# Performance work log

Measured on AMD Instinct MI355X. Metric: run time of the kernel, lower is better.

The kernel has to match this reference:

```python
import jax, jax.numpy as jnp
import numpy as np

EMBED_DIM = 1024
NUM_HEADS = 16
HEAD_DIM = EMBED_DIM // NUM_HEADS
B, S = 2, 2048


def setup_inputs() -> dict:
    key = jax.random.key(0)
    ks = jax.random.split(key, 11)
    sc = 1.0 / np.sqrt(EMBED_DIM)
    d = {
        'query': jax.random.normal(ks[0], (B, S, EMBED_DIM), jnp.float32),
        'key': jax.random.normal(ks[1], (B, S, EMBED_DIM), jnp.float32),
        'value': jax.random.normal(ks[2], (B, S, EMBED_DIM), jnp.float32),
        'Wq': jax.random.normal(ks[3], (EMBED_DIM, EMBED_DIM), jnp.float32) * sc,
        'bq': jnp.zeros((EMBED_DIM,), jnp.float32),
        'Wk': jax.random.normal(ks[4], (EMBED_DIM, EMBED_DIM), jnp.float32) * sc,
        'bk': jnp.zeros((EMBED_DIM,), jnp.float32),
        'Wv': jax.random.normal(ks[5], (EMBED_DIM, EMBED_DIM), jnp.float32) * sc,
        'bv': jnp.zeros((EMBED_DIM,), jnp.float32),
        'Wo': jax.random.normal(ks[6], (EMBED_DIM, EMBED_DIM), jnp.float32) * sc,
        'bo': jnp.zeros((EMBED_DIM,), jnp.float32),
    }
    return d


def reference(query, key, value, Wq, bq, Wk, bk, Wv, bv, Wo, bo):
    b, s, _ = query.shape
    scale = 1.0 / np.sqrt(HEAD_DIM)
    # projections: torch Linear is x @ W.T + b
    q = (query @ Wq.T + bq).reshape(b, s, NUM_HEADS, HEAD_DIM).transpose(0, 2, 1, 3)
    k = (key @ Wk.T + bk).reshape(b, s, NUM_HEADS, HEAD_DIM).transpose(0, 2, 1, 3)
    v = (value @ Wv.T + bv).reshape(b, s, NUM_HEADS, HEAD_DIM).transpose(0, 2, 1, 3)
    scores = jnp.einsum('bhqd,bhkd->bhqk', q, k) * scale  # [B,H,S,S]
    causal = jnp.triu(jnp.ones((s, s), bool), k=1)
    scores = jnp.where(causal, -jnp.inf, scores)
    attn = jax.nn.softmax(scores, axis=-1)
    out = jnp.einsum('bhqk,bhkd->bhqd', attn, v)
    out = out.transpose(0, 2, 1, 3).reshape(b, s, EMBED_DIM)
    out = out @ Wo.T + bo
    return out, attn
```

## Files before the change

kernel.cpp:

```cpp
#include <hip/hip_runtime.h>
#include <hip/hip_bf16.h>

#define BATCH  2
#define SEQ    2048
#define EMBED  1024
#define NHEADS 16
#define HDIM   64
#define SCALE  0.125f
#define S2     0.180336880f
#define MFIX   20.0f

typedef __attribute__((ext_vector_type(8))) short   short8;
typedef __attribute__((ext_vector_type(4))) float   floatx4;

#if __has_builtin(__builtin_amdgcn_exp2f)
#define EXP2(x) __builtin_amdgcn_exp2f(x)
#else
#define EXP2(x) exp2f(x)
#endif

#define GLOAD_LDS(g, l) __builtin_amdgcn_global_load_lds(                      \
    (const __attribute__((address_space(1))) void*)(const void*)(g),           \
    (__attribute__((address_space(3))) void*)(void*)(l), 16, 0, 0)

__device__ __forceinline__ float bf2f(unsigned short h) {
    union { unsigned int u; float f; } v; v.u = ((unsigned int)h) << 16; return v.f;
}
__device__ __forceinline__ unsigned short f2bf(float f) {
    union { float f; unsigned int u; } v; v.f = f;
    unsigned int r = v.u + 0x7FFF + ((v.u >> 16) & 1);
    return (unsigned short)(r >> 16);
}
__device__ __forceinline__ unsigned int pack2(float lo, float hi) {
    return (unsigned int)f2bf(lo) | ((unsigned int)f2bf(hi) << 16);
}

__global__ __launch_bounds__(256)
void cvt_bf16(const float* __restrict__ q,  const float* __restrict__ k,
              const float* __restrict__ v,  const float* __restrict__ wq,
              const float* __restrict__ wk, const float* __restrict__ wv,
              const float* __restrict__ wo,
              unsigned short* __restrict__ dq,  unsigned short* __restrict__ dk,
              unsigned short* __restrict__ dv,  unsigned short* __restrict__ dwq,
              unsigned short* __restrict__ dwk, unsigned short* __restrict__ dwv,
              unsigned short* __restrict__ dwo)
{
    const float* s; unsigned short* d; int n;
    switch (blockIdx.y) {
        case 0: s = q;  d = dq;  n = BATCH * SEQ * EMBED; break;
        case 1: s = k;  d = dk;  n = BATCH * SEQ * EMBED; break;
        case 2: s = v;  d = dv;  n = BATCH * SEQ * EMBED; break;
        case 3: s = wq; d = dwq; n = EMBED * EMBED; break;
        case 4: s = wk; d = dwk; n = EMBED * EMBED; break;
        case 5: s = wv; d = dwv; n = EMBED * EMBED; break;
        default: s = wo; d = dwo; n = EMBED * EMBED; break;
    }
    const int i = (blockIdx.x * 256 + threadIdx.x) * 8;
    if (i >= n) return;
    float4 f0 = ((const float4*)(s + i))[0];
    float4 f1 = ((const float4*)(s + i))[1];
    uint4 u = {pack2(f0.x, f0.y), pack2(f0.z, f0.w),
               pack2(f1.x, f1.y), pack2(f1.z, f1.w)};
    *(uint4*)(d + i) = u;
}

__device__ __forceinline__ void gemm_body(
    const unsigned short* __restrict__ A,
    const unsigned short* __restrict__ W,
    const float* __restrict__ bias,
    void* __restrict__ Cout, const int f32out)
{
    constexpr int M = BATCH * SEQ;
    constexpr int N = EMBED;
    constexpr int K = EMBED;

    __shared__ unsigned short As[2][128 * 64];
    __shared__ unsigned short Bs[2][64 * 64];

    const int t    = threadIdx.x;
    const int w    = t >> 6;
    const int lane = t & 63;
    const int lr   = lane & 15;
    const int quad = lane >> 4;
    const int n0   = blockIdx.x * 64;
    const int m0   = blockIdx.y * 128;

    size_t agoff[4];
    #pragma unroll
    for (int i = 0; i < 4; ++i) {
        const int slot = i * 256 + w * 64 + lane;
        const int row  = slot >> 3;
        const int g    = (slot & 7) ^ (row & 7);
        agoff[i] = (size_t)(m0 + row) * K + g * 8;
    }
    size_t bgoff[2];
    #pragma unroll
    for (int i = 0; i < 2; ++i) {
        const int slot = i * 256 + w * 64 + lane;
        const int row  = slot >> 3;
        const int g    = (slot & 7) ^ (row & 7);
        bgoff[i] = (size_t)(n0 + row) * K + g * 8;
    }

    int aoff[2][2], boff[4][2];
    #pragma unroll
    for (int mb = 0; mb < 2; ++mb)
        #pragma unroll
        for (int s = 0; s < 2; ++s) {
            const int row = w * 32 + mb * 16 + lr;
            aoff[mb][s] = row * 64 + (((s * 4 + quad) ^ (row & 7)) * 8);
        }
    #pragma unroll
    for (int nb = 0; nb < 4; ++nb)
        #pragma unroll
        for (int s = 0; s < 2; ++s) {
            const int row = nb * 16 + lr;
            boff[nb][s] = row * 64 + (((s * 4 + quad) ^ (row & 7)) * 8);
        }

    floatx4 acc[2][4];
    #pragma unroll
    for (int mb = 0; mb < 2; ++mb)
        #pragma unroll
        for (int nb = 0; nb < 4; ++nb) acc[mb][nb] = (floatx4){0.f, 0.f, 0.f, 0.f};

    auto stage = [&](int buf, int k0) {
        #pragma unroll
        for (int i = 0; i < 4; ++i)
            GLOAD_LDS(A + agoff[i] + k0, &As[buf][(i * 256 + w * 64) * 8]);
        #pragma unroll
        for (int i = 0; i < 2; ++i)
            GLOAD_LDS(W + bgoff[i] + k0, &Bs[buf][(i * 256 + w * 64) * 8]);
    };
    auto compute = [&](int buf) {
        const unsigned short* Ab = As[buf];
        const unsigned short* Bb = Bs[buf];
        #pragma unroll
        for (int s = 0; s < 2; ++s) {
            short8 a0 = *(const short8*)&Ab[aoff[0][s]];
            short8 a1 = *(const short8*)&Ab[aoff[1][s]];
            #pragma unroll
            for (int nb = 0; nb < 4; ++nb) {
                short8 bfr = *(const short8*)&Bb[boff[nb][s]];
                acc[0][nb] = __builtin_amdgcn_mfma_f32_16x16x32_bf16(a0, bfr, acc[0][nb], 0, 0, 0);
                acc[1][nb] = __builtin_amdgcn_mfma_f32_16x16x32_bf16(a1, bfr, acc[1][nb], 0, 0, 0);
            }
        }
    };

    stage(0, 0);
    __syncthreads();
    for (int k0 = 0; k0 < K; k0 += 128) {
        if (k0 + 64 < K) stage(1, k0 + 64);
        compute(0);
        __syncthreads();
        if (k0 + 128 < K) stage(0, k0 + 128);
        compute(1);
        __syncthreads();
    }

    #pragma unroll
    for (int mb = 0; mb < 2; ++mb)
        #pragma unroll
        for (int nb = 0; nb < 4; ++nb) {
            const int col = n0 + nb * 16 + lr;
            const float bv = bias[col];
            #pragma unroll
            for (int r = 0; r < 4; ++r) {
                const int row = m0 + w * 32 + mb * 16 + quad * 4 + r;
                const float val = acc[mb][nb][r] + bv;
                if (f32out) ((float*)Cout)[(size_t)row * N + col] = val;
                else        ((unsigned short*)Cout)[(size_t)row * N + col] = f2bf(val);
            }
        }
}

__global__ __launch_bounds__(256)
void gemm_qkv(const unsigned short* __restrict__ xq, const unsigned short* __restrict__ xk,
              const unsigned short* __restrict__ xv,
              const unsigned short* __restrict__ wq, const unsigned short* __restrict__ wk,
              const unsigned short* __restrict__ wv,
              const float* __restrict__ bq, const float* __restrict__ bk,
              const float* __restrict__ bv,
              unsigned short* __restrict__ Qb, unsigned short* __restrict__ Kb,
              unsigned short* __restrict__ Vb)
{
    const unsigned short *A, *W; const float* bias; unsigned short* C;
    switch (blockIdx.z) {
        case 0:  A = xq; W = wq; bias = bq; C = Qb; break;
        case 1:  A = xk; W = wk; bias = bk; C = Kb; break;
        default: A = xv; W = wv; bias = bv; C = Vb; break;
    }
    gemm_body(A, W, bias, C, 0);
}

__global__ __launch_bounds__(256)
void gemm_out(const unsigned short* __restrict__ A, const unsigned short* __restrict__ W,
              const float* __restrict__ bias, float* __restrict__ Cout)
{
    gemm_body(A, W, bias, Cout, 1);
}

__global__ __launch_bounds__(256)
void attn_fused(const unsigned short* __restrict__ Qb,
                const unsigned short* __restrict__ Kb,
                const unsigned short* __restrict__ Vb,
                float* __restrict__ attn,
                unsigned short* __restrict__ AO)
{
    __shared__ unsigned short Qs[64][72];
    __shared__ unsigned short Ks[64][72];
    __shared__ unsigned short Ps[64][72];
    __shared__ unsigned short Vt[64][72];

    const int t    = threadIdx.x;
    const int w    = t >> 6;
    const int lane = t & 63;
    const int lr   = lane & 15;
    const int quad = lane >> 4;
    const int qt   = blockIdx.x;
    const int h    = blockIdx.y;
    const int b    = blockIdx.z;
    const int q0   = qt * 64;
    const int srow = t >> 2;
    const int sseg = (t & 3) * 16;

    const size_t kvbase = (size_t)b * SEQ * EMBED + h * HDIM;
    const unsigned short* Krow = Kb + kvbase + (size_t)srow * EMBED + sseg;
    const unsigned short* Vrow = Vb + kvbase + (size_t)lane * EMBED;

    uint4 kra, krb;
    { const uint4* kp = (const uint4*)Krow; kra = kp[0]; krb = kp[1]; }

    {
        const uint4* qp = (const uint4*)(Qb + kvbase + (size_t)(q0 + srow) * EMBED + sseg);
        uint4 a0 = qp[0], a1 = qp[1];
        *(uint4*)&Qs[srow][sseg]     = a0;
        *(uint4*)&Qs[srow][sseg + 8] = a1;
    }

    float lsum[4];
    #pragma unroll
    for (int r = 0; r < 4; ++r) lsum[r] = 0.f;

    for (int kt = 0; kt <= qt; ++kt) {
        const int k0 = kt * 64;
        __syncthreads();
        *(uint4*)&Ks[srow][sseg]     = kra;
        *(uint4*)&Ks[srow][sseg + 8] = krb;
        if (kt < qt) {
            const uint4* kp = (const uint4*)(Krow + (size_t)(k0 + 64) * EMBED);
            kra = kp[0]; krb = kp[1];
        }
        __syncthreads();

        floatx4 sf[4];
        #pragma unroll
        for (int i = 0; i < 4; ++i) sf[i] = (floatx4){0.f, 0.f, 0.f, 0.f};
        #pragma unroll
        for (int s = 0; s < 2; ++s) {
            short8 af = *(const short8*)&Qs[w * 16 + lr][s * 32 + quad * 8];
            #pragma unroll
            for (int nb = 0; nb < 4; ++nb) {
                short8 bf = *(const short8*)&Ks[nb * 16 + lr][s * 32 + quad * 8];
                sf[nb] = __builtin_amdgcn_mfma_f32_16x16x32_bf16(af, bf, sf[nb], 0, 0, 0);
            }
        }

        #pragma unroll
        for (int r = 0; r < 4; ++r) {
            const int q = q0 + w * 16 + quad * 4 + r;
            #pragma unroll
            for (int nb = 0; nb < 4; ++nb) {
                const int k = k0 + nb * 16 + lr;
                float x = sf[nb][r] * S2 - MFIX;
                if (k > q) x = -200.f;
                lsum[r] += EXP2(x);
            }
        }
    }

    float invl[4];
    #pragma unroll
    for (int r = 0; r < 4; ++r) {
        #pragma unroll
        for (int off = 1; off < 16; off <<= 1)
            lsum[r] += __shfl_xor(lsum[r], off, 64);
        invl[r] = 1.f / lsum[r];
    }

    { const uint4* kp = (const uint4*)Krow; kra = kp[0]; krb = kp[1]; }
    uint4 vr0 = *(const uint4*)(Vrow + w * 8);
    uint4 vr1 = *(const uint4*)(Vrow + (w + 4) * 8);

    floatx4 of[4];
    #pragma unroll
    for (int i = 0; i < 4; ++i) of[i] = (floatx4){0.f, 0.f, 0.f, 0.f};

    float* attn_bh = attn + ((size_t)(b * NHEADS + h)) * SEQ * SEQ;

    for (int kt = 0; kt <= qt; ++kt) {
        const int k0 = kt * 64;
        __syncthreads();
        *(uint4*)&Ks[srow][sseg]     = kra;
        *(uint4*)&Ks[srow][sseg + 8] = krb;
        {
            const unsigned short* pv0 = (const unsigned short*)&vr0;
            const unsigned short* pv1 = (const unsigned short*)&vr1;
            #pragma unroll
            for (int j = 0; j < 8; ++j) Vt[w * 8 + j][lane]       = pv0[j];
            #pragma unroll
            for (int j = 0; j < 8; ++j) Vt[(w + 4) * 8 + j][lane] = pv1[j];
        }
        if (kt < qt) {
            const uint4* kp = (const uint4*)(Krow + (size_t)(k0 + 64) * EMBED);
            kra = kp[0]; krb = kp[1];
            vr0 = *(const uint4*)(Vrow + (size_t)(k0 + 64) * EMBED + w * 8);
            vr1 = *(const uint4*)(Vrow + (size_t)(k0 + 64) * EMBED + (w + 4) * 8);
        }
        __syncthreads();

        floatx4 sf[4];
        #pragma unroll
        for (int i = 0; i < 4; ++i) sf[i] = (floatx4){0.f, 0.f, 0.f, 0.f};
        #pragma unroll
        for (int s = 0; s < 2; ++s) {
            short8 af = *(const short8*)&Qs[w * 16 + lr][s * 32 + quad * 8];
            #pragma unroll
            for (int nb = 0; nb < 4; ++nb) {
                short8 bf = *(const short8*)&Ks[nb * 16 + lr][s * 32 + quad * 8];
                sf[nb] = __builtin_amdgcn_mfma_f32_16x16x32_bf16(af, bf, sf[nb], 0, 0, 0);
            }
        }

        #pragma unroll
        for (int nb = 0; nb < 4; ++nb) {
            const int k = k0 + nb * 16 + lr;
            #pragma unroll
            for (int r = 0; r < 4; ++r) {
                const int q = q0 + w * 16 + quad * 4 + r;
                float p = 0.f;
                if (k <= q) p = EXP2(sf[nb][r] * S2 - MFIX) * invl[r];
                Ps[w * 16 + quad * 4 + r][nb * 16 + lr] = f2bf(p);
            }
        }
        __syncthreads();

        {
            const unsigned short* ps = &Ps[srow][sseg];
            float* op = attn_bh + (size_t)(q0 + srow) * SEQ + k0 + sseg;
            #pragma unroll
            for (int g = 0; g < 4; ++g) {
                float4 f;
                f.x = bf2f(ps[g * 4 + 0]);
                f.y = bf2f(ps[g * 4 + 1]);
                f.z = bf2f(ps[g * 4 + 2]);
                f.w = bf2f(ps[g * 4 + 3]);
                ((float4*)op)[g] = f;
            }
        }

        #pragma unroll
        for (int s = 0; s < 2; ++s) {
            short8 af = *(const short8*)&Ps[w * 16 + lr][s * 32 + quad * 8];
            #pragma unroll
            for (int nb = 0; nb < 4; ++nb) {
                short8 bf = *(const short8*)&Vt[nb * 16 + lr][s * 32 + quad * 8];
                of[nb] = __builtin_amdgcn_mfma_f32_16x16x32_bf16(af, bf, of[nb], 0, 0, 0);
            }
        }
    }

    for (int kt = qt + 1; kt < SEQ / 64; ++kt) {
        float4 z = {0.f, 0.f, 0.f, 0.f};
        float* op = attn_bh + (size_t)(q0 + srow) * SEQ + kt * 64 + sseg;
        #pragma unroll
        for (int g = 0; g < 4; ++g) ((float4*)op)[g] = z;
    }

    #pragma unroll
    for (int nb = 0; nb < 4; ++nb) {
        #pragma unroll
        for (int r = 0; r < 4; ++r) {
            const int q = q0 + w * 16 + quad * 4 + r;
            const int d = nb * 16 + lr;
            AO[(size_t)(b * SEQ + q) * EMBED + h * HDIM + d] = f2bf(of[nb][r]);
        }
    }
}

extern "C" void kernel_launch(void* const* d_in, const int* in_sizes, int n_in,
                              void* d_out, int out_size, void* d_ws, size_t ws_size,
                              hipStream_t stream)
{
    const float* query = (const float*)d_in[0];
    const float* key   = (const float*)d_in[1];
    const float* value = (const float*)d_in[2];
    const float* Wq    = (const float*)d_in[3];
    const float* bq    = (const float*)d_in[4];
    const float* Wk    = (const float*)d_in[5];
    const float* bk    = (const float*)d_in[6];
    const float* Wv    = (const float*)d_in[7];
    const float* bv    = (const float*)d_in[8];
    const float* Wo    = (const float*)d_in[9];
    const float* bo    = (const float*)d_in[10];

    float* out  = (float*)d_out;
    float* attn = out + (size_t)BATCH * SEQ * EMBED;

    const size_t tsz = (size_t)BATCH * SEQ * EMBED;
    const size_t wsz = (size_t)EMBED * EMBED;
    unsigned short* p = (unsigned short*)d_ws;
    unsigned short* xq  = p;  p += tsz;
    unsigned short* xk  = p;  p += tsz;
    unsigned short* xv  = p;  p += tsz;
    unsigned short* wq16 = p; p += wsz;
    unsigned short* wk16 = p; p += wsz;
    unsigned short* wv16 = p; p += wsz;
    unsigned short* wo16 = p; p += wsz;
    unsigned short* Qb  = p;  p += tsz;
    unsigned short* Kb  = p;  p += tsz;
    unsigned short* Vb  = p;  p += tsz;
    unsigned short* AO  = p;  p += tsz;

    const dim3 blk(256);

    cvt_bf16<<<dim3(2048, 7), blk, 0, stream>>>(query, key, value, Wq, Wk, Wv, Wo,
                                                xq, xk, xv, wq16, wk16, wv16, wo16);

    const dim3 gqkv(EMBED / 64, (BATCH * SEQ) / 128, 3);
    gemm_qkv<<<gqkv, blk, 0, stream>>>(xq, xk, xv, wq16, wk16, wv16,
                                       bq, bk, bv, Qb, Kb, Vb);

    attn_fused<<<dim3(SEQ / 64, NHEADS, BATCH), blk, 0, stream>>>(Qb, Kb, Vb, attn, AO);

    const dim3 gout(EMBED / 64, (BATCH * SEQ) / 128);
    gemm_out<<<gout, blk, 0, stream>>>(AO, wo16, bo, out);
}
```

Baseline: 798.9 us.

## Load Q/K MFMA fragments directly from global, double-buffer V, cut barriers in attention

```diff
diff --git a/kernel.cpp b/kernel.cpp
--- a/kernel.cpp
+++ b/kernel.cpp
@@ -9,6 +9,7 @@
 #define SCALE  0.125f
 #define S2     0.180336880f
 #define MFIX   20.0f
+#define PPITCH 88
 
 typedef __attribute__((ext_vector_type(8))) short   short8;
 typedef __attribute__((ext_vector_type(4))) float   floatx4;
@@ -33,6 +34,13 @@
 }
 __device__ __forceinline__ unsigned int pack2(float lo, float hi) {
     return (unsigned int)f2bf(lo) | ((unsigned int)f2bf(hi) << 16);
+}
+
+__device__ __forceinline__ void bar_lds() {
+    __builtin_amdgcn_sched_barrier(0);
+    asm volatile("s_waitcnt lgkmcnt(0)" ::: "memory");
+    __builtin_amdgcn_s_barrier();
+    __builtin_amdgcn_sched_barrier(0);
 }
 
 __global__ __launch_bounds__(256)
@@ -70,7 +78,6 @@
     const float* __restrict__ bias,
     void* __restrict__ Cout, const int f32out)
 {
-    constexpr int M = BATCH * SEQ;
     constexpr int N = EMBED;
     constexpr int K = EMBED;
 
@@ -208,74 +215,75 @@
                 float* __restrict__ attn,
                 unsigned short* __restrict__ AO)
 {
-    __shared__ unsigned short Qs[64][72];
-    __shared__ unsigned short Ks[64][72];
-    __shared__ unsigned short Ps[64][72];
-    __shared__ unsigned short Vt[64][72];
+    __shared__ unsigned short Ps[64][PPITCH];
+    __shared__ unsigned short Vt[2][64][PPITCH];
 
     const int t    = threadIdx.x;
     const int w    = t >> 6;
     const int lane = t & 63;
     const int lr   = lane & 15;
     const int quad = lane >> 4;
-    const int qt   = blockIdx.x;
     const int h    = blockIdx.y;
     const int b    = blockIdx.z;
+    const int slot = (h >> 3) + 2 * b;
+    const int qt   = (slot & 1) ? (SEQ / 64 - 1 - (int)blockIdx.x) : (int)blockIdx.x;
     const int q0   = qt * 64;
     const int srow = t >> 2;
     const int sseg = (t & 3) * 16;
 
     const size_t kvbase = (size_t)b * SEQ * EMBED + h * HDIM;
-    const unsigned short* Krow = Kb + kvbase + (size_t)srow * EMBED + sseg;
-    const unsigned short* Vrow = Vb + kvbase + (size_t)lane * EMBED;
-
-    uint4 kra, krb;
-    { const uint4* kp = (const uint4*)Krow; kra = kp[0]; krb = kp[1]; }
-
-    {
-        const uint4* qp = (const uint4*)(Qb + kvbase + (size_t)(q0 + srow) * EMBED + sseg);
-        uint4 a0 = qp[0], a1 = qp[1];
-        *(uint4*)&Qs[srow][sseg]     = a0;
-        *(uint4*)&Qs[srow][sseg + 8] = a1;
-    }
+
+    const unsigned short* qrow = Qb + kvbase + (size_t)(q0 + w * 16 + lr) * EMBED + quad * 8;
+    const short8 af0 = *(const short8*)(qrow);
+    const short8 af1 = *(const short8*)(qrow + 32);
+
+    const unsigned short* kfrag = Kb + kvbase + (size_t)lr * EMBED + quad * 8;
+    const unsigned short* Vrow  = Vb + kvbase + (size_t)lane * EMBED;
 
     float lsum[4];
     #pragma unroll
     for (int r = 0; r < 4; ++r) lsum[r] = 0.f;
 
     for (int kt = 0; kt <= qt; ++kt) {
-        const int k0 = kt * 64;
-        __syncthreads();
-        *(uint4*)&Ks[srow][sseg]     = kra;
-        *(uint4*)&Ks[srow][sseg + 8] = krb;
+        const unsigned short* kp = kfrag + (size_t)(kt * 64) * EMBED;
+        short8 kb0[4], kb1[4];
+        #pragma unroll
+        for (int nb = 0; nb < 4; ++nb) kb0[nb] = *(const short8*)(kp + (size_t)(nb * 16) * EMBED);
+        #pragma unroll
+        for (int nb = 0; nb < 4; ++nb) kb1[nb] = *(const short8*)(kp + (size_t)(nb * 16) * EMBED + 32);
+
+        floatx4 sf[4];
+        #pragma unroll
+        for (int i = 0; i < 4; ++i) sf[i] = (floatx4){0.f, 0.f, 0.f, 0.f};
+        #pragma unroll
+        for (int nb = 0; nb < 4; ++nb)
+            sf[nb] = __builtin_amdgcn_mfma_f32_16x16x32_bf16(af0, kb0[nb], sf[nb], 0, 0, 0);
+        #pragma unroll
+        for (int nb = 0; nb < 4; ++nb)
+            sf[nb] = __builtin_amdgcn_mfma_f32_16x16x32_bf16(af1, kb1[nb], sf[nb], 0, 0, 0);
+
         if (kt < qt) {
-            const uint4* kp = (const uint4*)(Krow + (size_t)(k0 + 64) * EMBED);
-            kra = kp[0]; krb = kp[1];
-        }
-        __syncthreads();
-
-        floatx4 sf[4];
-        #pragma unroll
-        for (int i = 0; i < 4; ++i) sf[i] = (floatx4){0.f, 0.f, 0.f, 0.f};
-        #pragma unroll
-        for (int s = 0; s < 2; ++s) {
-            short8 af = *(const short8*)&Qs[w * 16 + lr][s * 32 + quad * 8];
-            #pragma unroll
-            for (int nb = 0; nb < 4; ++nb) {
-                short8 bf = *(const short8*)&Ks[nb * 16 + lr][s * 32 + quad * 8];
-                sf[nb] = __builtin_amdgcn_mfma_f32_16x16x32_bf16(af, bf, sf[nb], 0, 0, 0);
-            }
-        }
-
-        #pragma unroll
-        for (int r = 0; r < 4; ++r) {
-            const int q = q0 + w * 16 + quad * 4 + r;
-            #pragma unroll
-            for (int nb = 0; nb < 4; ++nb) {
-                const int k = k0 + nb * 16 + lr;
-                float x = sf[nb][r] * S2 - MFIX;
-                if (k > q) x = -200.f;
-                lsum[r] += EXP2(x);
+            #pragma unroll
+            for (int r = 0; r < 4; ++r) {
+                float e0 = EXP2(sf[0][r] * S2 - MFIX);
+                float e1 = EXP2(sf[1][r] * S2 - MFIX);
+                float e2 = EXP2(sf[2][r] * S2 - MFIX);
+                float e3 = EXP2(sf[3][r] * S2 - MFIX);
+                lsum[r] += (e0 + e1) + (e2 + e3);
+            }
+        } else {
+            #pragma unroll
+            for (int r = 0; r < 4; ++r) {
+                const int q = w * 16 + quad * 4 + r;
+                float e[4];
+                #pragma unroll
+                for (int nb = 0; nb < 4; ++nb) {
+                    const int k = nb * 16 + lr;
+                    float x = sf[nb][r] * S2 - MFIX;
+                    if (k > q) x = -1e30f;
+                    e[nb] = EXP2(x);
+                }
+                lsum[r] += (e[0] + e[1]) + (e[2] + e[3]);
             }
         }
     }
@@ -289,66 +297,87 @@
         invl[r] = 1.f / lsum[r];
     }
 
-    { const uint4* kp = (const uint4*)Krow; kra = kp[0]; krb = kp[1]; }
-    uint4 vr0 = *(const uint4*)(Vrow + w * 8);
-    uint4 vr1 = *(const uint4*)(Vrow + (w + 4) * 8);
-
     floatx4 of[4];
     #pragma unroll
     for (int i = 0; i < 4; ++i) of[i] = (floatx4){0.f, 0.f, 0.f, 0.f};
 
     float* attn_bh = attn + ((size_t)(b * NHEADS + h)) * SEQ * SEQ;
+
+    auto stageVt = [&](int buf, const uint4& a, const uint4& bb) {
+        const unsigned short* pv0 = (const unsigned short*)&a;
+        const unsigned short* pv1 = (const unsigned short*)&bb;
+        #pragma unroll
+        for (int j = 0; j < 8; ++j) Vt[buf][w * 8 + j][lane]       = pv0[j];
+        #pragma unroll
+        for (int j = 0; j < 8; ++j) Vt[buf][(w + 4) * 8 + j][lane] = pv1[j];
+    };
+
+    uint4 va  = *(const uint4*)(Vrow + w * 8);
+    uint4 vb2 = *(const uint4*)(Vrow + (w + 4) * 8);
+    stageVt(0, va, vb2);
+    if (qt > 0) {
+        va  = *(const uint4*)(Vrow + (size_t)64 * EMBED + w * 8);
+        vb2 = *(const uint4*)(Vrow + (size_t)64 * EMBED + (w + 4) * 8);
+    }
+    bar_lds();
 
     for (int kt = 0; kt <= qt; ++kt) {
         const int k0 = kt * 64;
-        __syncthreads();
-        *(uint4*)&Ks[srow][sseg]     = kra;
-        *(uint4*)&Ks[srow][sseg + 8] = krb;
+
+        const unsigned short* kp = kfrag + (size_t)k0 * EMBED;
+        short8 kb0[4], kb1[4];
+        #pragma unroll
+        for (int nb = 0; nb < 4; ++nb) kb0[nb] = *(const short8*)(kp + (size_t)(nb * 16) * EMBED);
+        #pragma unroll
+        for (int nb = 0; nb < 4; ++nb) kb1[nb] = *(const short8*)(kp + (size_t)(nb * 16) * EMBED + 32);
+
+        if (kt) bar_lds();
+
+        if (kt < qt) {
+            stageVt((kt + 1) & 1, va, vb2);
+            if (kt + 2 <= qt) {
+                va  = *(const uint4*)(Vrow + (size_t)(k0 + 128) * EMBED + w * 8);
+                vb2 = *(const uint4*)(Vrow + (size_t)(k0 + 128) * EMBED + (w + 4) * 8);
+            }
+        }
+
+        floatx4 sf[4];
+        #pragma unroll
+        for (int i = 0; i < 4; ++i) sf[i] = (floatx4){0.f, 0.f, 0.f, 0.f};
+        #pragma unroll
+        for (int nb = 0; nb < 4; ++nb)
+            sf[nb] = __builtin_amdgcn_mfma_f32_16x16x32_bf16(af0, kb0[nb], sf[nb], 0, 0, 0);
+        #pragma unroll
+        for (int nb = 0; nb < 4; ++nb)
+            sf[nb] = __builtin_amdgcn_mfma_f32_16x16x32_bf16(af1, kb1[nb], sf[nb], 0, 0, 0);
+
+        if (kt < qt) {
+            #pragma unroll
+            for (int nb = 0; nb < 4; ++nb)
+                #pragma unroll
+                for (int r = 0; r < 4; ++r) {
+                    float p = EXP2(sf[nb][r] * S2 - MFIX) * invl[r];
+                    Ps[w * 16 + quad * 4 + r][nb * 16 + lr] = f2bf(p);
+                }
+        } else {
+            #pragma unroll
+            for (int nb = 0; nb < 4; ++nb) {
+                const int k = nb * 16 + lr;
+                #pragma unroll
+                for (int r = 0; r < 4; ++r) {
+                    const int q = w * 16 + quad * 4 + r;
+                    float p = 0.f;
+                    if (k <= q) p = EXP2(sf[nb][r] * S2 - MFIX) * invl[r];
+                    Ps[w * 16 + quad * 4 + r][nb * 16 + lr] = f2bf(p);
+                }
+            }
+        }
+
         {
-            const unsigned short* pv0 = (const unsigned short*)&vr0;
-            const unsigned short* pv1 = (const unsigned short*)&vr1;
-            #pragma unroll
-            for (int j = 0; j < 8; ++j) Vt[w * 8 + j][lane]       = pv0[j];
-            #pragma unroll
-            for (int j = 0; j < 8; ++j) Vt[(w + 4) * 8 + j][lane] = pv1[j];
-        }
-        if (kt < qt) {
-            const uint4* kp = (const uint4*)(Krow + (size_t)(k0 + 64) * EMBED);
-            kra = kp[0]; krb = kp[1];
-            vr0 = *(const uint4*)(Vrow + (size_t)(k0 + 64) * EMBED + w * 8);
-            vr1 = *(const uint4*)(Vrow + (size_t)(k0 + 64) * EMBED + (w + 4) * 8);
-        }
-        __syncthreads();
-
-        floatx4 sf[4];
-        #pragma unroll
-        for (int i = 0; i < 4; ++i) sf[i] = (floatx4){0.f, 0.f, 0.f, 0.f};
-        #pragma unroll
-        for (int s = 0; s < 2; ++s) {
-            short8 af = *(const short8*)&Qs[w * 16 + lr][s * 32 + quad * 8];
-            #pragma unroll
-            for (int nb = 0; nb < 4; ++nb) {
-                short8 bf = *(const short8*)&Ks[nb * 16 + lr][s * 32 + quad * 8];
-                sf[nb] = __builtin_amdgcn_mfma_f32_16x16x32_bf16(af, bf, sf[nb], 0, 0, 0);
-            }
-        }
-
-        #pragma unroll
-        for (int nb = 0; nb < 4; ++nb) {
-            const int k = k0 + nb * 16 + lr;
-            #pragma unroll
-            for (int r = 0; r < 4; ++r) {
-                const int q = q0 + w * 16 + quad * 4 + r;
-                float p = 0.f;
-                if (k <= q) p = EXP2(sf[nb][r] * S2 - MFIX) * invl[r];
-                Ps[w * 16 + quad * 4 + r][nb * 16 + lr] = f2bf(p);
-            }
-        }
-        __syncthreads();
-
-        {
-            const unsigned short* ps = &Ps[srow][sseg];
-            float* op = attn_bh + (size_t)(q0 + srow) * SEQ + k0 + sseg;
+            const int rrow = lane >> 2;
+            const int rseg = (lane & 3) * 16;
+            const unsigned short* ps = &Ps[w * 16 + rrow][rseg];
+            float* op = attn_bh + (size_t)(q0 + w * 16 + rrow) * SEQ + k0 + rseg;
             #pragma unroll
             for (int g = 0; g < 4; ++g) {
                 float4 f;
@@ -362,11 +391,11 @@
 
         #pragma unroll
         for (int s = 0; s < 2; ++s) {
-            short8 af = *(const short8*)&Ps[w * 16 + lr][s * 32 + quad * 8];
+            short8 paf = *(const short8*)&Ps[w * 16 + lr][s * 32 + quad * 8];
             #pragma unroll
             for (int nb = 0; nb < 4; ++nb) {
-                short8 bf = *(const short8*)&Vt[nb * 16 + lr][s * 32 + quad * 8];
-                of[nb] = __builtin_amdgcn_mfma_f32_16x16x32_bf16(af, bf, of[nb], 0, 0, 0);
+                short8 vf = *(const short8*)&Vt[kt & 1][nb * 16 + lr][s * 32 + quad * 8];
+                of[nb] = __builtin_amdgcn_mfma_f32_16x16x32_bf16(paf, vf, of[nb], 0, 0, 0);
             }
         }
     }
@@ -379,13 +408,16 @@
     }
 
     #pragma unroll
-    for (int nb = 0; nb < 4; ++nb) {
-        #pragma unroll
-        for (int r = 0; r < 4; ++r) {
-            const int q = q0 + w * 16 + quad * 4 + r;
-            const int d = nb * 16 + lr;
-            AO[(size_t)(b * SEQ + q) * EMBED + h * HDIM + d] = f2bf(of[nb][r]);
-        }
+    for (int nb = 0; nb < 4; ++nb)
+        #pragma unroll
+        for (int r = 0; r < 4; ++r)
+            Ps[w * 16 + quad * 4 + r][nb * 16 + lr] = f2bf(of[nb][r]);
+    {
+        const int rrow = lane >> 2;
+        const int rseg = (lane & 3) * 16;
+        unsigned short* ao = AO + (size_t)(b * SEQ + q0 + w * 16 + rrow) * EMBED + h * HDIM + rseg;
+        *(uint4*)ao       = *(const uint4*)&Ps[w * 16 + rrow][rseg];
+        *(uint4*)(ao + 8) = *(const uint4*)&Ps[w * 16 + rrow][rseg + 8];
     }
 }
 
```

After: 835.4 us. 1.05x slower.
